# Optimization experiments

Hardware: AMD Instinct MI355X
Metric: run time of the kernel (lower is better)

## Reference

```python
import jax, jax.numpy as jnp
import numpy as np

N_NODES = 50000
N_EDGES = 300000
HEADS = 2
OUT_CH = 128
BN_EPS = 1e-5
NEG_SLOPE = 0.2


def _batchnorm(x, g, b):
    # training-mode BatchNorm1d: biased batch statistics
    mean = x.mean(axis=0)
    var = x.var(axis=0)
    return (x - mean) * jax.lax.rsqrt(var + BN_EPS) * g + b


def _gatv2(x, src, dst, edge_attr, Wl, bl, Wr, br, We, att, bias, concat):
    # PyG GATv2Conv, share_weights=False, aggr='add'
    n = x.shape[0]
    xl = (x @ Wl + bl).reshape(n, HEADS, OUT_CH)  # source messages
    xr = (x @ Wr + br).reshape(n, HEADS, OUT_CH)  # destination term
    ee = (edge_attr @ We).reshape(-1, HEADS, OUT_CH)
    s = jax.nn.leaky_relu(xl[src] + xr[dst] + ee, NEG_SLOPE)  # [E,H,C]
    alpha = jnp.einsum('ehc,hc->eh', s, att)  # [E,H]
    # segment softmax over edges grouped by destination node
    m = jax.ops.segment_max(alpha, dst, num_segments=n)
    a = jnp.exp(alpha - m[dst])
    den = jax.ops.segment_sum(a, dst, num_segments=n)
    a = a / (den[dst] + 1e-16)
    out = jax.ops.segment_sum(xl[src] * a[:, :, None], dst, num_segments=n)  # [N,H,C]
    out = out.reshape(n, HEADS * OUT_CH) if concat else out.mean(axis=1)
    return out + bias


def setup_inputs() -> dict:
    key = jax.random.key(0)
    ks = jax.random.split(key, 16)
    d = {}
    d['h'] = jax.random.normal(ks[0], (N_NODES, 5), jnp.float32)
    d['edge_index'] = jax.random.randint(ks[1], (2, N_EDGES), 0, N_NODES, jnp.int64)
    d['edge_weight'] = jax.random.uniform(ks[2], (N_EDGES, 1), jnp.float32)
    d['bn0_g'] = jnp.ones((5,), jnp.float32)
    d['bn0_b'] = jnp.zeros((5,), jnp.float32)
    d['bn1_g'] = jnp.ones((256,), jnp.float32)
    d['bn1_b'] = jnp.zeros((256,), jnp.float32)
    def lin(k, fan_in, fan_out):
        return jax.random.normal(k, (fan_in, fan_out), jnp.float32) * (1.0 / np.sqrt(fan_in))
    # conv1: in=5 -> heads*out=256, concat=True
    d['c1_Wl'] = lin(ks[3], 5, 256); d['c1_bl'] = jnp.zeros((256,), jnp.float32)
    d['c1_Wr'] = lin(ks[4], 5, 256); d['c1_br'] = jnp.zeros((256,), jnp.float32)
    d['c1_We'] = lin(ks[5], 1, 256)
    d['c1_att'] = jax.random.normal(ks[6], (HEADS, OUT_CH), jnp.float32) * 0.1
    d['c1_bias'] = jnp.zeros((256,), jnp.float32)
    # mu: in=256 -> 128, concat=False
    d['mu_Wl'] = lin(ks[7], 256, 256); d['mu_bl'] = jnp.zeros((256,), jnp.float32)
    d['mu_Wr'] = lin(ks[8], 256, 256); d['mu_br'] = jnp.zeros((256,), jnp.float32)
    d['mu_We'] = lin(ks[9], 1, 256)
    d['mu_att'] = jax.random.normal(ks[10], (HEADS, OUT_CH), jnp.float32) * 0.1
    d['mu_bias'] = jnp.zeros((128,), jnp.float32)
    # log_std: same shapes as mu
    d['ls_Wl'] = lin(ks[11], 256, 256); d['ls_bl'] = jnp.zeros((256,), jnp.float32)
    d['ls_Wr'] = lin(ks[12], 256, 256); d['ls_br'] = jnp.zeros((256,), jnp.float32)
    d['ls_We'] = lin(ks[13], 1, 256)
    d['ls_att'] = jax.random.normal(ks[14], (HEADS, OUT_CH), jnp.float32) * 0.1
    d['ls_bias'] = jnp.zeros((128,), jnp.float32)
    return d


def reference(h, edge_index, edge_weight, bn0_g, bn0_b, bn1_g, bn1_b,
              c1_Wl, c1_bl, c1_Wr, c1_br, c1_We, c1_att, c1_bias,
              mu_Wl, mu_bl, mu_Wr, mu_br, mu_We, mu_att, mu_bias,
              ls_Wl, ls_bl, ls_Wr, ls_br, ls_We, ls_att, ls_bias):
    src, dst = edge_index[0], edge_index[1]
    x = _batchnorm(h, bn0_g, bn0_b)
    x = _gatv2(x, src, dst, edge_weight, c1_Wl, c1_bl, c1_Wr, c1_br, c1_We, c1_att, c1_bias, concat=True)
    x = jax.nn.relu(_batchnorm(x, bn1_g, bn1_b))
    # dropout identity (eval / deterministic)
    mu = _gatv2(x, src, dst, edge_weight, mu_Wl, mu_bl, mu_Wr, mu_br, mu_We, mu_att, mu_bias, concat=False)
    log_std = _gatv2(x, src, dst, edge_weight, ls_Wl, ls_bl, ls_Wr, ls_br, ls_We, ls_att, ls_bias, concat=False)
    return (mu, log_std)
```

## Files before the change

### kernel.cpp

```cpp
#include <hip/hip_runtime.h>
#include <math.h>

#define N_NODES 50000
#define N_EDGES 300000
#define BN_EPS 1e-5f
#define NEG_SLOPE 0.2f

#define RB_COUNT 3128
#define SCAN_TILES 49
#define BN1_BLOCKS 523
#define K5_BLOCKS 1024

#define PREP_BN0 128
#define PREP_EC  1172
#define PREP_PW  128

typedef short bf8v __attribute__((ext_vector_type(8)));
typedef float f4v __attribute__((ext_vector_type(4)));
typedef float f2v __attribute__((ext_vector_type(2)));

__device__ inline unsigned short f2bf(float f) {
    union { float f; unsigned u; } c; c.f = f;
    unsigned r = c.u + 0x7fffu + ((c.u >> 16) & 1u);
    return (unsigned short)(r >> 16);
}

__device__ inline f2v bfpair(unsigned u) {
    union { unsigned u; float f; } lo, hi;
    lo.u = u << 16;
    hi.u = u & 0xffff0000u;
    f2v r; r.x = lo.f; r.y = hi.f;
    return r;
}

__device__ inline void async_copy16(void* lds, const void* g) {
    __builtin_amdgcn_global_load_lds(
        (const __attribute__((address_space(1))) unsigned int*)g,
        (__attribute__((address_space(3))) unsigned int*)lds, 16, 0, 0);
}

__global__ __launch_bounds__(256) void prep(
        const float* __restrict__ h, float* __restrict__ acc,
        const int* __restrict__ dst, int* __restrict__ count,
        const float* __restrict__ Wl0, const float* __restrict__ Wr0,
        const float* __restrict__ Wl1, const float* __restrict__ Wr1,
        unsigned short* __restrict__ bp) {
    int b = blockIdx.x;
    if (b < PREP_BN0) {
        __shared__ float lds[4][10];
        int tid = threadIdx.x;
        int lane = tid & 63, wave = tid >> 6;
        float ls[5] = {0,0,0,0,0}, lq[5] = {0,0,0,0,0};
        for (int r = b * 256 + tid; r < N_NODES; r += PREP_BN0 * 256) {
            #pragma unroll
            for (int k = 0; k < 5; k++) {
                float v = h[r*5 + k];
                ls[k] += v; lq[k] += v*v;
            }
        }
        #pragma unroll
        for (int k = 0; k < 5; k++) {
            #pragma unroll
            for (int m = 1; m <= 32; m <<= 1) {
                ls[k] += __shfl_xor(ls[k], m, 64);
                lq[k] += __shfl_xor(lq[k], m, 64);
            }
        }
        if (lane == 0) {
            #pragma unroll
            for (int k = 0; k < 5; k++) { lds[wave][k] = ls[k]; lds[wave][5+k] = lq[k]; }
        }
        __syncthreads();
        if (tid < 10) {
            float s = lds[0][tid] + lds[1][tid] + lds[2][tid] + lds[3][tid];
            atomicAdd(&acc[tid], s);
        }
    } else if (b < PREP_BN0 + PREP_EC) {
        int e = (b - PREP_BN0) * 256 + threadIdx.x;
        if (e < N_EDGES) atomicAdd(&count[dst[e]], 1);
    } else {
        int t = (b - PREP_BN0 - PREP_EC) * 256 + threadIdx.x;
        int lane = t & 63;
        int nt = (t >> 6) & 31;
        int kc = (t >> 11) & 7;
        int conv = t >> 14;
        int col = nt * 16 + (lane & 15);
        int k0 = kc * 32 + (lane >> 4) * 8;
        const float* W = conv ? (col < 256 ? Wl1 : Wr1) : (col < 256 ? Wl0 : Wr0);
        int c = col & 255;
        union { unsigned short h[8]; uint4 u; } tmp;
        #pragma unroll
        for (int j = 0; j < 8; j++) tmp.h[j] = f2bf(W[(size_t)(k0 + j) * 256 + c]);
        *reinterpret_cast<uint4*>(bp + (size_t)t * 8) = tmp.u;
    }
}

__global__ void local_scan(const int* __restrict__ count, int* __restrict__ offsets,
                           int* __restrict__ tileSum) {
    __shared__ int wsum[16];
    int tid = threadIdx.x;
    int lane = tid & 63, wv = tid >> 6;
    int i = blockIdx.x * 1024 + tid;
    int v = (i < N_NODES) ? count[i] : 0;
    int inc = v;
    #pragma unroll
    for (int off = 1; off < 64; off <<= 1) {
        int t = __shfl_up(inc, off, 64);
        if (lane >= off) inc += t;
    }
    if (lane == 63) wsum[wv] = inc;
    __syncthreads();
    if (wv == 0) {
        int val = (lane < 16) ? wsum[lane] : 0;
        int inc2 = val;
        #pragma unroll
        for (int off = 1; off < 16; off <<= 1) {
            int t = __shfl_up(inc2, off, 64);
            if (lane >= off) inc2 += t;
        }
        if (lane < 16) wsum[lane] = inc2 - val;
    }
    __syncthreads();
    int excl = inc - v + wsum[wv];
    if (i < N_NODES) offsets[i] = excl;
    if (tid == 1023) tileSum[blockIdx.x] = excl + v;
}

__global__ void add_prefix(int* __restrict__ offsets, const int* __restrict__ tileSum,
                           int* __restrict__ cursor) {
    __shared__ int spref;
    int tid = threadIdx.x;
    if (tid < 64) {
        int v = (tid < blockIdx.x) ? tileSum[tid] : 0;
        #pragma unroll
        for (int m = 1; m <= 32; m <<= 1) v += __shfl_xor(v, m, 64);
        if (tid == 0) spref = v;
    }
    __syncthreads();
    int i = blockIdx.x * 1024 + tid;
    if (i < N_NODES) {
        int o = offsets[i] + spref;
        offsets[i] = o;
        cursor[i] = o;
    }
    if (blockIdx.x == 0 && tid == 0) offsets[N_NODES] = N_EDGES;
}

__global__ void edge_scatter(const int* __restrict__ dst, const int* __restrict__ src,
                             const float* __restrict__ ew, int* __restrict__ cursor,
                             int2* __restrict__ sep) {
    int e = blockIdx.x * blockDim.x + threadIdx.x;
    if (e < N_EDGES) {
        int pos = atomicAdd(&cursor[dst[e]], 1);
        sep[pos] = make_int2(src[e], __float_as_int(ew[e]));
    }
}

__global__ __launch_bounds__(128) void gemm_k5(const float* __restrict__ h,
        const float* __restrict__ acc10, const float* __restrict__ g5,
        const float* __restrict__ b5,
        const float* __restrict__ Wl, const float* __restrict__ bl,
        const float* __restrict__ Wr, const float* __restrict__ br,
        unsigned short* __restrict__ xl, unsigned short* __restrict__ xr) {
    int c = threadIdx.x * 2;
    float sc[5], sh[5];
    #pragma unroll
    for (int k = 0; k < 5; k++) {
        float mean = acc10[k] * (1.f / N_NODES);
        float var  = acc10[5 + k] * (1.f / N_NODES) - mean * mean;
        float s = g5[k] * rsqrtf(var + BN_EPS);
        sc[k] = s; sh[k] = b5[k] - mean * s;
    }
    float wl0[5], wl1[5], wr0[5], wr1[5];
    #pragma unroll
    for (int k = 0; k < 5; k++) {
        wl0[k] = Wl[k*256 + c]; wl1[k] = Wl[k*256 + c + 1];
        wr0[k] = Wr[k*256 + c]; wr1[k] = Wr[k*256 + c + 1];
    }
    float bl0 = bl[c], bl1 = bl[c+1], br0 = br[c], br1 = br[c+1];
    int n = blockIdx.x;
    float hv[5];
    if (n < N_NODES) {
        #pragma unroll
        for (int k = 0; k < 5; k++) hv[k] = h[n*5 + k];
    }
    for (; n < N_NODES; n += K5_BLOCKS) {
        int n2 = n + K5_BLOCKS;
        float hn[5] = {0,0,0,0,0};
        if (n2 < N_NODES) {
            #pragma unroll
            for (int k = 0; k < 5; k++) hn[k] = h[n2*5 + k];
        }
        float l0 = bl0, l1 = bl1, r0 = br0, r1 = br1;
        #pragma unroll
        for (int k = 0; k < 5; k++) {
            float a = hv[k] * sc[k] + sh[k];
            l0 += a * wl0[k]; l1 += a * wl1[k];
            r0 += a * wr0[k]; r1 += a * wr1[k];
        }
        unsigned lp = (unsigned)f2bf(l0) | ((unsigned)f2bf(l1) << 16);
        unsigned rp = (unsigned)f2bf(r0) | ((unsigned)f2bf(r1) << 16);
        *reinterpret_cast<unsigned*>(xl + (size_t)n*256 + c) = lp;
        *reinterpret_cast<unsigned*>(xr + (size_t)n*256 + c) = rp;
        #pragma unroll
        for (int k = 0; k < 5; k++) hv[k] = hn[k];
    }
}

__global__ void pack_x_bn(const unsigned short* __restrict__ xh, const float* __restrict__ ss1,
                          unsigned short* __restrict__ ap) {
    int t = blockIdx.x * 256 + threadIdx.x;
    int lane = t & 63;
    int kc = (t >> 6) & 7;
    int rb = t >> 9;
    int row = rb * 16 + (lane & 15);
    int k0 = kc * 32 + (lane >> 4) * 8;
    union { unsigned short h[8]; uint4 u; } tmp;
    if (row < N_NODES) {
        uint4 u = *(const uint4*)(xh + (size_t)row * 256 + k0);
        float f[8];
        f2v p;
        p = bfpair(u.x); f[0] = p.x; f[1] = p.y;
        p = bfpair(u.y); f[2] = p.x; f[3] = p.y;
        p = bfpair(u.z); f[4] = p.x; f[5] = p.y;
        p = bfpair(u.w); f[6] = p.x; f[7] = p.y;
        #pragma unroll
        for (int j = 0; j < 8; j++) {
            int cc = k0 + j;
            float v = f[j] * ss1[cc] + ss1[256 + cc];
            v = v > 0.f ? v : 0.f;
            tmp.h[j] = f2bf(v);
        }
    } else {
        #pragma unroll
        for (int j = 0; j < 8; j++) tmp.h[j] = 0;
    }
    *reinterpret_cast<uint4*>(ap + (size_t)t * 8) = tmp.u;
}

__global__ __launch_bounds__(512) void gemm_mfma(const unsigned short* __restrict__ ap,
        const unsigned short* __restrict__ bp,
        const float* __restrict__ bl0, const float* __restrict__ br0,
        const float* __restrict__ bl1, const float* __restrict__ br1,
        unsigned short* __restrict__ xlA, unsigned short* __restrict__ xrA,
        unsigned short* __restrict__ xlB, unsigned short* __restrict__ xrB) {
    __shared__ unsigned short Bs[2][32][512];
    int cv = blockIdx.x >= 782;
    int bb = cv ? blockIdx.x - 782 : blockIdx.x;
    int lane = threadIdx.x & 63;
    int wave = threadIdx.x >> 6;
    int h = wave & 1;
    int rb = bb * 4 + (wave >> 1);

    const unsigned short* aptr = ap + (size_t)rb * 4096 + lane * 8;
    const unsigned short* bsrc = bp + (size_t)cv * 131072 + lane * 8;

    auto stage = [&](int buf, int kc) {
        #pragma unroll
        for (int j = 0; j < 4; j++) {
            int f = wave * 4 + j;
            async_copy16(&Bs[buf][f][lane * 8], bsrc + (size_t)kc * 16384 + f * 512);
        }
    };
    stage(0, 0);

    bf8v a[8];
    #pragma unroll
    for (int kc = 0; kc < 8; kc++) a[kc] = *reinterpret_cast<const bf8v*>(aptr + kc * 512);

    f4v acc[16];
    #pragma unroll
    for (int t = 0; t < 16; t++) acc[t] = (f4v){0.f, 0.f, 0.f, 0.f};

    for (int kc = 0; kc < 8; kc++) {
        __syncthreads();
        if (kc < 7) stage((kc + 1) & 1, kc + 1);
        const unsigned short* bb2 = &Bs[kc & 1][h * 16][lane * 8];
        #pragma unroll
        for (int t = 0; t < 16; t++) {
            bf8v b = *reinterpret_cast<const bf8v*>(bb2 + t * 512);
            acc[t] = __builtin_amdgcn_mfma_f32_16x16x32_bf16(a[kc], b, acc[t], 0, 0, 0);
        }
    }

    int c15 = lane & 15;
    int row0 = rb * 16 + (lane >> 4) * 4;
    unsigned short* outp = cv ? (h ? xrB : xlB) : (h ? xrA : xlA);
    const float* bias = cv ? (h ? br1 : bl1) : (h ? br0 : bl0);
    #pragma unroll
    for (int t = 0; t < 16; t++) {
        int col = t * 16 + c15;
        float bv = bias[col];
        #pragma unroll
        for (int r = 0; r < 4; r++) {
            int row = row0 + r;
            if (row < N_NODES) outp[(size_t)row * 256 + col] = f2bf(acc[t][r] + bv);
        }
    }
}

__global__ __launch_bounds__(256) void agg_concat(
        const unsigned short* __restrict__ xl, const unsigned short* __restrict__ xr,
        const float* __restrict__ We, const float* __restrict__ att,
        const int* __restrict__ offsets, const int2* __restrict__ sep,
        const float* __restrict__ bias,
        unsigned short* __restrict__ outh) {
    int n = blockIdx.x * 4 + (threadIdx.x >> 6);
    int lane = threadIdx.x & 63;
    int half = lane >> 5;
    int sub  = lane & 31;
    int cb   = (sub >> 4) * 128 + (sub & 15) * 8;
    f2v wv[4], av[4], rv[4];
    {
        f4v t0 = *(const f4v*)(We + cb);
        f4v t1 = *(const f4v*)(We + cb + 4);
        wv[0] = (f2v){t0.x, t0.y}; wv[1] = (f2v){t0.z, t0.w};
        wv[2] = (f2v){t1.x, t1.y}; wv[3] = (f2v){t1.z, t1.w};
        t0 = *(const f4v*)(att + cb);
        t1 = *(const f4v*)(att + cb + 4);
        av[0] = (f2v){t0.x, t0.y}; av[1] = (f2v){t0.z, t0.w};
        av[2] = (f2v){t1.x, t1.y}; av[3] = (f2v){t1.z, t1.w};
        uint4 r8 = *(const uint4*)(xr + ((size_t)n << 8) + cb);
        rv[0] = bfpair(r8.x); rv[1] = bfpair(r8.y);
        rv[2] = bfpair(r8.z); rv[3] = bfpair(r8.w);
    }
    int beg = offsets[n], end = offsets[n + 1];
    float den = 0.f;
    f2v acc[4];
    #pragma unroll
    for (int j = 0; j < 4; j++) acc[j] = (f2v){0.f, 0.f};

    int i = beg + half;
    float wN = 0.f;
    int2 seP = make_int2(0, 0);
    uint4 lN = {0u, 0u, 0u, 0u};
    if (i < end) {
        int2 se = sep[i];
        wN = __int_as_float(se.y);
        lN = *(const uint4*)(xl + ((size_t)se.x << 8) + cb);
    }
    if (i + 2 < end) seP = sep[i + 2];
    for (; i < end; i += 2) {
        uint4 l8 = lN; float w = wN;
        if (i + 2 < end) {
            lN = *(const uint4*)(xl + ((size_t)seP.x << 8) + cb);
            wN = __int_as_float(seP.y);
        }
        if (i + 4 < end) seP = sep[i + 4];
        f2v w2 = (f2v){w, w};
        f2v lv[4];
        lv[0] = bfpair(l8.x); lv[1] = bfpair(l8.y);
        lv[2] = bfpair(l8.z); lv[3] = bfpair(l8.w);
        f2v da = (f2v){0.f, 0.f};
        #pragma unroll
        for (int j = 0; j < 4; j++) {
            f2v v = lv[j] + rv[j] + w2 * wv[j];
            f2v s = v * (f2v){NEG_SLOPE, NEG_SLOPE};
            v.x = fmaxf(v.x, s.x); v.y = fmaxf(v.y, s.y);
            da += v * av[j];
        }
        float a = da.x + da.y;
        a += __shfl_xor(a, 1, 64);
        a += __shfl_xor(a, 2, 64);
        a += __shfl_xor(a, 4, 64);
        a += __shfl_xor(a, 8, 64);
        float p = __expf(a);
        den += p;
        f2v p2 = (f2v){p, p};
        #pragma unroll
        for (int j = 0; j < 4; j++) acc[j] += p2 * lv[j];
    }
    den += __shfl_xor(den, 32, 64);
    #pragma unroll
    for (int j = 0; j < 4; j++) {
        f2v ao;
        ao.x = __shfl_xor(acc[j].x, 32, 64);
        ao.y = __shfl_xor(acc[j].y, 32, 64);
        acc[j] += ao;
    }
    float inv = 1.f / (den + 1e-16f);
    if (lane < 32) {
        union { unsigned short hh[8]; uint4 u; } o;
        #pragma unroll
        for (int j = 0; j < 4; j++) {
            o.hh[2*j]   = f2bf(acc[j].x * inv + bias[cb + 2*j]);
            o.hh[2*j+1] = f2bf(acc[j].y * inv + bias[cb + 2*j + 1]);
        }
        *(uint4*)(outh + (size_t)n * 256 + cb) = o.u;
    }
}

__global__ __launch_bounds__(256) void agg_dual(
        const unsigned short* __restrict__ xlA, const unsigned short* __restrict__ xrA,
        const unsigned short* __restrict__ xlB, const unsigned short* __restrict__ xrB,
        const float* __restrict__ WeA, const float* __restrict__ attA,
        const float* __restrict__ WeB, const float* __restrict__ attB,
        const int* __restrict__ offsets, const int2* __restrict__ sep,
        const float* __restrict__ biasA, const float* __restrict__ biasB,
        float* __restrict__ outA, float* __restrict__ outB) {
    int n = blockIdx.x * 4 + (threadIdx.x >> 6);
    int lane = threadIdx.x & 63;
    int half = lane >> 5;
    int sub  = lane & 31;
    int cb   = (sub >> 4) * 128 + (sub & 15) * 8;
    f2v wvA[4], avA[4], rvA[4], wvB[4], avB[4], rvB[4];
    {
        f4v t0 = *(const f4v*)(WeA + cb);
        f4v t1 = *(const f4v*)(WeA + cb + 4);
        wvA[0] = (f2v){t0.x, t0.y}; wvA[1] = (f2v){t0.z, t0.w};
        wvA[2] = (f2v){t1.x, t1.y}; wvA[3] = (f2v){t1.z, t1.w};
        t0 = *(const f4v*)(attA + cb);
        t1 = *(const f4v*)(attA + cb + 4);
        avA[0] = (f2v){t0.x, t0.y}; avA[1] = (f2v){t0.z, t0.w};
        avA[2] = (f2v){t1.x, t1.y}; avA[3] = (f2v){t1.z, t1.w};
        t0 = *(const f4v*)(WeB + cb);
        t1 = *(const f4v*)(WeB + cb + 4);
        wvB[0] = (f2v){t0.x, t0.y}; wvB[1] = (f2v){t0.z, t0.w};
        wvB[2] = (f2v){t1.x, t1.y}; wvB[3] = (f2v){t1.z, t1.w};
        t0 = *(const f4v*)(attB + cb);
        t1 = *(const f4v*)(attB + cb + 4);
        avB[0] = (f2v){t0.x, t0.y}; avB[1] = (f2v){t0.z, t0.w};
        avB[2] = (f2v){t1.x, t1.y}; avB[3] = (f2v){t1.z, t1.w};
        uint4 r8 = *(const uint4*)(xrA + ((size_t)n << 8) + cb);
        rvA[0] = bfpair(r8.x); rvA[1] = bfpair(r8.y);
        rvA[2] = bfpair(r8.z); rvA[3] = bfpair(r8.w);
        r8 = *(const uint4*)(xrB + ((size_t)n << 8) + cb);
        rvB[0] = bfpair(r8.x); rvB[1] = bfpair(r8.y);
        rvB[2] = bfpair(r8.z); rvB[3] = bfpair(r8.w);
    }
    int beg = offsets[n], end = offsets[n + 1];
    float dA = 0.f, dB = 0.f;
    f2v accA[4], accB[4];
    #pragma unroll
    for (int j = 0; j < 4; j++) { accA[j] = (f2v){0.f, 0.f}; accB[j] = (f2v){0.f, 0.f}; }

    int i = beg + half;
    float wN = 0.f;
    int2 seP = make_int2(0, 0);
    uint4 lNA = {0u, 0u, 0u, 0u}, lNB = {0u, 0u, 0u, 0u};
    if (i < end) {
        int2 se = sep[i];
        wN = __int_as_float(se.y);
        size_t o = ((size_t)se.x << 8) + cb;
        lNA = *(const uint4*)(xlA + o);
        lNB = *(const uint4*)(xlB + o);
    }
    if (i + 2 < end) seP = sep[i + 2];
    for (; i < end; i += 2) {
        uint4 lA = lNA, lB = lNB; float w = wN;
        if (i + 2 < end) {
            size_t o = ((size_t)seP.x << 8) + cb;
            lNA = *(const uint4*)(xlA + o);
            lNB = *(const uint4*)(xlB + o);
            wN = __int_as_float(seP.y);
        }
        if (i + 4 < end) seP = sep[i + 4];
        f2v w2 = (f2v){w, w};
        f2v lvA[4], lvB[4];
        lvA[0] = bfpair(lA.x); lvA[1] = bfpair(lA.y);
        lvA[2] = bfpair(lA.z); lvA[3] = bfpair(lA.w);
        lvB[0] = bfpair(lB.x); lvB[1] = bfpair(lB.y);
        lvB[2] = bfpair(lB.z); lvB[3] = bfpair(lB.w);
        f2v daA = (f2v){0.f, 0.f}, daB = (f2v){0.f, 0.f};
        #pragma unroll
        for (int j = 0; j < 4; j++) {
            f2v vA = lvA[j] + rvA[j] + w2 * wvA[j];
            f2v sA = vA * (f2v){NEG_SLOPE, NEG_SLOPE};
            vA.x = fmaxf(vA.x, sA.x); vA.y = fmaxf(vA.y, sA.y);
            daA += vA * avA[j];
            f2v vB = lvB[j] + rvB[j] + w2 * wvB[j];
            f2v sB = vB * (f2v){NEG_SLOPE, NEG_SLOPE};
            vB.x = fmaxf(vB.x, sB.x); vB.y = fmaxf(vB.y, sB.y);
            daB += vB * avB[j];
        }
        float aA = daA.x + daA.y, aB = daB.x + daB.y;
        float tA, tB;
        tA = __shfl_xor(aA, 1, 64); tB = __shfl_xor(aB, 1, 64); aA += tA; aB += tB;
        tA = __shfl_xor(aA, 2, 64); tB = __shfl_xor(aB, 2, 64); aA += tA; aB += tB;
        tA = __shfl_xor(aA, 4, 64); tB = __shfl_xor(aB, 4, 64); aA += tA; aB += tB;
        tA = __shfl_xor(aA, 8, 64); tB = __shfl_xor(aB, 8, 64); aA += tA; aB += tB;
        float pA = __expf(aA), pB = __expf(aB);
        dA += pA; dB += pB;
        f2v pA2 = (f2v){pA, pA}, pB2 = (f2v){pB, pB};
        #pragma unroll
        for (int j = 0; j < 4; j++) {
            accA[j] += pA2 * lvA[j];
            accB[j] += pB2 * lvB[j];
        }
    }
    dA += __shfl_xor(dA, 32, 64);
    dB += __shfl_xor(dB, 32, 64);
    #pragma unroll
    for (int j = 0; j < 4; j++) {
        f2v ao;
        ao.x = __shfl_xor(accA[j].x, 32, 64);
        ao.y = __shfl_xor(accA[j].y, 32, 64);
        accA[j] += ao;
        ao.x = __shfl_xor(accB[j].x, 32, 64);
        ao.y = __shfl_xor(accB[j].y, 32, 64);
        accB[j] += ao;
    }
    float invA = 1.f / (dA + 1e-16f);
    float invB = 1.f / (dB + 1e-16f);
    float oA[8], oB[8], poA[8], poB[8];
    #pragma unroll
    for (int j = 0; j < 4; j++) {
        oA[2*j]   = accA[j].x * invA;
        oA[2*j+1] = accA[j].y * invA;
        oB[2*j]   = accB[j].x * invB;
        oB[2*j+1] = accB[j].y * invB;
    }
    #pragma unroll
    for (int j = 0; j < 8; j++) {
        poA[j] = __shfl_xor(oA[j], 16, 64);
        poB[j] = __shfl_xor(oB[j], 16, 64);
    }
    int q = lane >> 4;
    int c0 = (lane & 15) * 8;
    if (q == 0) {
        float r[8];
        #pragma unroll
        for (int j = 0; j < 8; j++) r[j] = (oA[j] + poA[j]) * 0.5f + biasA[c0 + j];
        *(float4*)(outA + (size_t)n * 128 + c0)     = *(float4*)&r[0];
        *(float4*)(outA + (size_t)n * 128 + c0 + 4) = *(float4*)&r[4];
    } else if (q == 2) {
        float r[8];
        #pragma unroll
        for (int j = 0; j < 8; j++) r[j] = (oB[j] + poB[j]) * 0.5f + biasB[c0 + j];
        *(float4*)(outB + (size_t)n * 128 + c0)     = *(float4*)&r[0];
        *(float4*)(outB + (size_t)n * 128 + c0 + 4) = *(float4*)&r[4];
    }
}

__global__ void bn1_reduce(const unsigned short* __restrict__ xh, float* __restrict__ part) {
    __shared__ float lds[256][9];
    int tid = threadIdx.x;
    int cg = tid & 63;
    int ph = tid >> 6;
    int r0 = blockIdx.x * 96;
    float s[4] = {0,0,0,0}, q[4] = {0,0,0,0};
    #pragma unroll
    for (int it = 0; it < 24; it++) {
        int row = r0 + it * 4 + ph;
        if (row < N_NODES) {
            uint2 v = *(const uint2*)(xh + (size_t)row * 256 + cg * 4);
            f2v p0 = bfpair(v.x), p1 = bfpair(v.y);
            s[0] += p0.x; s[1] += p0.y; s[2] += p1.x; s[3] += p1.y;
            q[0] += p0.x*p0.x; q[1] += p0.y*p0.y; q[2] += p1.x*p1.x; q[3] += p1.y*p1.y;
        }
    }
    #pragma unroll
    for (int j = 0; j < 4; j++) { lds[tid][j] = s[j]; lds[tid][4+j] = q[j]; }
    __syncthreads();
    if (tid < 64) {
        float4 sv, qv;
        float* svp = (float*)&sv; float* qvp = (float*)&qv;
        #pragma unroll
        for (int j = 0; j < 4; j++) {
            svp[j] = lds[tid][j] + lds[tid+64][j] + lds[tid+128][j] + lds[tid+192][j];
            qvp[j] = lds[tid][4+j] + lds[tid+64][4+j] + lds[tid+128][4+j] + lds[tid+192][4+j];
        }
        *(float4*)(part + (size_t)blockIdx.x * 512 + cg * 4) = sv;
        *(float4*)(part + (size_t)blockIdx.x * 512 + 256 + cg * 4) = qv;
    }
}

__global__ void bn1_finalize(const float* __restrict__ part, const float* __restrict__ g,
                             const float* __restrict__ b, float* __restrict__ ss1) {
    __shared__ float lds[8][64];
    int t = threadIdx.x;
    int c = blockIdx.x * 32 + (t & 31);
    int ph = t >> 5;
    float s = 0.f, q = 0.f;
    for (int bi = ph; bi < BN1_BLOCKS; bi += 8) {
        s += part[(size_t)bi * 512 + c];
        q += part[(size_t)bi * 512 + 256 + c];
    }
    lds[ph][t & 31] = s;
    lds[ph][32 + (t & 31)] = q;
    __syncthreads();
    if (t < 32) {
        float ss = 0.f, qq = 0.f;
        #pragma unroll
        for (int p = 0; p < 8; p++) { ss += lds[p][t]; qq += lds[p][32 + t]; }
        float mean = ss * (1.f / N_NODES);
        float var  = qq * (1.f / N_NODES) - mean * mean;
        float sc = g[c] * rsqrtf(var + BN_EPS);
        ss1[c] = sc;
        ss1[256 + c] = b[c] - mean * sc;
    }
}

extern "C" void kernel_launch(void* const* d_in, const int* in_sizes, int n_in,
                              void* d_out, int out_size, void* d_ws, size_t ws_size,
                              hipStream_t stream) {
    const float* h          = (const float*)d_in[0];
    const int*   edge_index = (const int*)d_in[1];
    const int*   src = edge_index;
    const int*   dst = edge_index + N_EDGES;
    const float* ew   = (const float*)d_in[2];
    const float* bn0g = (const float*)d_in[3];
    const float* bn0b = (const float*)d_in[4];
    const float* bn1g = (const float*)d_in[5];
    const float* bn1b = (const float*)d_in[6];
    const float* c1_Wl = (const float*)d_in[7];
    const float* c1_bl = (const float*)d_in[8];
    const float* c1_Wr = (const float*)d_in[9];
    const float* c1_br = (const float*)d_in[10];
    const float* c1_We = (const float*)d_in[11];
    const float* c1_att = (const float*)d_in[12];
    const float* c1_bias = (const float*)d_in[13];
    const float* mu_Wl = (const float*)d_in[14];
    const float* mu_bl = (const float*)d_in[15];
    const float* mu_Wr = (const float*)d_in[16];
    const float* mu_br = (const float*)d_in[17];
    const float* mu_We = (const float*)d_in[18];
    const float* mu_att = (const float*)d_in[19];
    const float* mu_bias = (const float*)d_in[20];
    const float* ls_Wl = (const float*)d_in[21];
    const float* ls_bl = (const float*)d_in[22];
    const float* ls_Wr = (const float*)d_in[23];
    const float* ls_br = (const float*)d_in[24];
    const float* ls_We = (const float*)d_in[25];
    const float* ls_att = (const float*)d_in[26];
    const float* ls_bias = (const float*)d_in[27];

    float* out_mu = (float*)d_out;
    float* out_ls = (float*)d_out + (size_t)N_NODES * 128;

    char* ws = (char*)d_ws;
    size_t off = 0;
    auto alloc = [&](size_t bytes) -> void* {
        void* p = ws + off;
        off += (bytes + 255) / 256 * 256;
        return p;
    };
    unsigned short* xl = (unsigned short*)alloc((size_t)N_NODES * 256 * 2);
    unsigned short* xr = (unsigned short*)alloc((size_t)N_NODES * 256 * 2);
    unsigned short* xBh = (unsigned short*)alloc((size_t)N_NODES * 256 * 2);
    unsigned short* xr2 = (unsigned short*)alloc((size_t)N_NODES * 256 * 2);
    float* bn0acc  = (float*)alloc(10 * 4);
    float* bn1part = (float*)alloc((size_t)BN1_BLOCKS * 512 * 4);
    float* bn1ss   = (float*)alloc(512 * 4);
    int*   count   = (int*)alloc((size_t)N_NODES * 4);
    int*   offsets = (int*)alloc((size_t)(N_NODES + 1) * 4);
    int*   cursor  = (int*)alloc((size_t)N_NODES * 4);
    int2*  sep     = (int2*)alloc((size_t)N_EDGES * 8);
    int*   tileSum = (int*)alloc((size_t)SCAN_TILES * 4);
    unsigned short* Apack = (unsigned short*)alloc((size_t)RB_COUNT * 4096 * 2);
    unsigned short* Bpack = (unsigned short*)alloc((size_t)2 * 131072 * 2);

    unsigned short* xl2 = xBh;

    hipMemsetAsync(count, 0, (size_t)N_NODES * 4, stream);
    hipMemsetAsync(bn0acc, 0, 10 * 4, stream);

    prep<<<PREP_BN0 + PREP_EC + PREP_PW, 256, 0, stream>>>(
        h, bn0acc, dst, count, mu_Wl, mu_Wr, ls_Wl, ls_Wr, Bpack);

    local_scan<<<SCAN_TILES, 1024, 0, stream>>>(count, offsets, tileSum);
    add_prefix<<<SCAN_TILES, 1024, 0, stream>>>(offsets, tileSum, cursor);
    edge_scatter<<<(N_EDGES + 255) / 256, 256, 0, stream>>>(dst, src, ew, cursor, sep);

    gemm_k5<<<K5_BLOCKS, 128, 0, stream>>>(h, bn0acc, bn0g, bn0b,
                                           c1_Wl, c1_bl, c1_Wr, c1_br, xl, xr);
    agg_concat<<<N_NODES / 4, 256, 0, stream>>>(xl, xr, c1_We, c1_att, offsets,
                                                sep, c1_bias, xBh);

    bn1_reduce<<<BN1_BLOCKS, 256, 0, stream>>>(xBh, bn1part);
    bn1_finalize<<<8, 256, 0, stream>>>(bn1part, bn1g, bn1b, bn1ss);
    pack_x_bn<<<6256, 256, 0, stream>>>(xBh, bn1ss, Apack);

    gemm_mfma<<<1564, 512, 0, stream>>>(Apack, Bpack,
                                        mu_bl, mu_br, ls_bl, ls_br,
                                        xl, xr, xl2, xr2);

    agg_dual<<<N_NODES / 4, 256, 0, stream>>>(xl, xr, xl2, xr2,
                                              mu_We, mu_att, ls_We, ls_att,
                                              offsets, sep,
                                              mu_bias, ls_bias, out_mu, out_ls);
}
```

Measured before the change: 418.1 us.

## Fuse BN1+ReLU packing into MFMA GEMM and make aggregation kernels persistent

Removes the pack_x_bn kernel and its Apack buffer. The GEMM now reads the bf16 hidden activations directly, applies the BN1 scale/shift and ReLU in registers to build the A fragments, and computes both the mu and log_std projections in a single block so each A tile is loaded once. The aggregation kernels switch to a grid-stride persistent form with 2048 blocks, hoisting the bias loads and prefetching the next node's offsets. Because xl2 no longer aliases xBh it gets its own allocation, which uses more workspace. Halving the GEMM grid also lowers parallelism.

```diff
diff --git a/kernel.cpp b/kernel.cpp
--- a/kernel.cpp
+++ b/kernel.cpp
@@ -10,6 +10,9 @@
 #define SCAN_TILES 49
 #define BN1_BLOCKS 523
 #define K5_BLOCKS 1024
+
+#define AGG_BLOCKS 2048
+#define AGG_STRIDE (AGG_BLOCKS * 4)
 
 #define PREP_BN0 128
 #define PREP_EC  1172
@@ -207,94 +210,94 @@
     }
 }
 
-__global__ void pack_x_bn(const unsigned short* __restrict__ xh, const float* __restrict__ ss1,
-                          unsigned short* __restrict__ ap) {
-    int t = blockIdx.x * 256 + threadIdx.x;
-    int lane = t & 63;
-    int kc = (t >> 6) & 7;
-    int rb = t >> 9;
-    int row = rb * 16 + (lane & 15);
-    int k0 = kc * 32 + (lane >> 4) * 8;
-    union { unsigned short h[8]; uint4 u; } tmp;
-    if (row < N_NODES) {
-        uint4 u = *(const uint4*)(xh + (size_t)row * 256 + k0);
-        float f[8];
-        f2v p;
-        p = bfpair(u.x); f[0] = p.x; f[1] = p.y;
-        p = bfpair(u.y); f[2] = p.x; f[3] = p.y;
-        p = bfpair(u.z); f[4] = p.x; f[5] = p.y;
-        p = bfpair(u.w); f[6] = p.x; f[7] = p.y;
-        #pragma unroll
-        for (int j = 0; j < 8; j++) {
-            int cc = k0 + j;
-            float v = f[j] * ss1[cc] + ss1[256 + cc];
-            v = v > 0.f ? v : 0.f;
-            tmp.h[j] = f2bf(v);
-        }
-    } else {
-        #pragma unroll
-        for (int j = 0; j < 8; j++) tmp.h[j] = 0;
-    }
-    *reinterpret_cast<uint4*>(ap + (size_t)t * 8) = tmp.u;
-}
-
-__global__ __launch_bounds__(512) void gemm_mfma(const unsigned short* __restrict__ ap,
+__global__ __launch_bounds__(512) void gemm_mfma(const unsigned short* __restrict__ xh,
+        const float* __restrict__ ss1,
         const unsigned short* __restrict__ bp,
         const float* __restrict__ bl0, const float* __restrict__ br0,
         const float* __restrict__ bl1, const float* __restrict__ br1,
         unsigned short* __restrict__ xlA, unsigned short* __restrict__ xrA,
         unsigned short* __restrict__ xlB, unsigned short* __restrict__ xrB) {
     __shared__ unsigned short Bs[2][32][512];
-    int cv = blockIdx.x >= 782;
-    int bb = cv ? blockIdx.x - 782 : blockIdx.x;
     int lane = threadIdx.x & 63;
     int wave = threadIdx.x >> 6;
     int h = wave & 1;
-    int rb = bb * 4 + (wave >> 1);
-
-    const unsigned short* aptr = ap + (size_t)rb * 4096 + lane * 8;
-    const unsigned short* bsrc = bp + (size_t)cv * 131072 + lane * 8;
-
-    auto stage = [&](int buf, int kc) {
-        #pragma unroll
-        for (int j = 0; j < 4; j++) {
-            int f = wave * 4 + j;
-            async_copy16(&Bs[buf][f][lane * 8], bsrc + (size_t)kc * 16384 + f * 512);
-        }
-    };
-    stage(0, 0);
-
+    int rb = blockIdx.x * 4 + (wave >> 1);
+
+    int row = rb * 16 + (lane & 15);
+    int k0b = (lane >> 4) * 8;
+    bool rok = row < N_NODES;
     bf8v a[8];
     #pragma unroll
-    for (int kc = 0; kc < 8; kc++) a[kc] = *reinterpret_cast<const bf8v*>(aptr + kc * 512);
-
-    f4v acc[16];
-    #pragma unroll
-    for (int t = 0; t < 16; t++) acc[t] = (f4v){0.f, 0.f, 0.f, 0.f};
-
     for (int kc = 0; kc < 8; kc++) {
-        __syncthreads();
-        if (kc < 7) stage((kc + 1) & 1, kc + 1);
-        const unsigned short* bb2 = &Bs[kc & 1][h * 16][lane * 8];
-        #pragma unroll
-        for (int t = 0; t < 16; t++) {
-            bf8v b = *reinterpret_cast<const bf8v*>(bb2 + t * 512);
-            acc[t] = __builtin_amdgcn_mfma_f32_16x16x32_bf16(a[kc], b, acc[t], 0, 0, 0);
-        }
+        int k0 = kc * 32 + k0b;
+        union { unsigned short hh[8]; uint4 u; bf8v v; } tmp;
+        if (rok) {
+            uint4 u = *(const uint4*)(xh + (size_t)row * 256 + k0);
+            f4v s0 = *(const f4v*)(ss1 + k0);
+            f4v s1 = *(const f4v*)(ss1 + k0 + 4);
+            f4v h0 = *(const f4v*)(ss1 + 256 + k0);
+            f4v h1 = *(const f4v*)(ss1 + 256 + k0 + 4);
+            float f[8];
+            f2v p;
+            p = bfpair(u.x); f[0] = p.x; f[1] = p.y;
+            p = bfpair(u.y); f[2] = p.x; f[3] = p.y;
+            p = bfpair(u.z); f[4] = p.x; f[5] = p.y;
+            p = bfpair(u.w); f[6] = p.x; f[7] = p.y;
+            float scv[8] = {s0.x, s0.y, s0.z, s0.w, s1.x, s1.y, s1.z, s1.w};
+            float shv[8] = {h0.x, h0.y, h0.z, h0.w, h1.x, h1.y, h1.z, h1.w};
+            #pragma unroll
+            for (int j = 0; j < 8; j++) {
+                float v = f[j] * scv[j] + shv[j];
+                v = v > 0.f ? v : 0.f;
+                tmp.hh[j] = f2bf(v);
+            }
+        } else {
+            tmp.u = (uint4){0u, 0u, 0u, 0u};
+        }
+        a[kc] = tmp.v;
     }
 
     int c15 = lane & 15;
     int row0 = rb * 16 + (lane >> 4) * 4;
-    unsigned short* outp = cv ? (h ? xrB : xlB) : (h ? xrA : xlA);
-    const float* bias = cv ? (h ? br1 : bl1) : (h ? br0 : bl0);
+
     #pragma unroll
-    for (int t = 0; t < 16; t++) {
-        int col = t * 16 + c15;
-        float bv = bias[col];
-        #pragma unroll
-        for (int r = 0; r < 4; r++) {
-            int row = row0 + r;
-            if (row < N_NODES) outp[(size_t)row * 256 + col] = f2bf(acc[t][r] + bv);
+    for (int cv = 0; cv < 2; cv++) {
+        const unsigned short* bsrc = bp + (size_t)cv * 131072 + lane * 8;
+        auto stage = [&](int buf, int kc) {
+            #pragma unroll
+            for (int j = 0; j < 4; j++) {
+                int f = wave * 4 + j;
+                async_copy16(&Bs[buf][f][lane * 8], bsrc + (size_t)kc * 16384 + f * 512);
+            }
+        };
+        stage(0, 0);
+
+        f4v acc[16];
+        #pragma unroll
+        for (int t = 0; t < 16; t++) acc[t] = (f4v){0.f, 0.f, 0.f, 0.f};
+
+        for (int kc = 0; kc < 8; kc++) {
+            __syncthreads();
+            if (kc < 7) stage((kc + 1) & 1, kc + 1);
+            const unsigned short* bb2 = &Bs[kc & 1][h * 16][lane * 8];
+            #pragma unroll
+            for (int t = 0; t < 16; t++) {
+                bf8v b = *reinterpret_cast<const bf8v*>(bb2 + t * 512);
+                acc[t] = __builtin_amdgcn_mfma_f32_16x16x32_bf16(a[kc], b, acc[t], 0, 0, 0);
+            }
+        }
+
+        unsigned short* outp = cv ? (h ? xrB : xlB) : (h ? xrA : xlA);
+        const float* bias = cv ? (h ? br1 : bl1) : (h ? br0 : bl0);
+        #pragma unroll
+        for (int t = 0; t < 16; t++) {
+            int col = t * 16 + c15;
+            float bv = bias[col];
+            #pragma unroll
+            for (int r = 0; r < 4; r++) {
+                int rr = row0 + r;
+                if (rr < N_NODES) outp[(size_t)rr * 256 + col] = f2bf(acc[t][r] + bv);
+            }
         }
     }
 }
@@ -305,12 +308,13 @@
         const int* __restrict__ offsets, const int2* __restrict__ sep,
         const float* __restrict__ bias,
         unsigned short* __restrict__ outh) {
-    int n = blockIdx.x * 4 + (threadIdx.x >> 6);
+    int gw = blockIdx.x * 4 + (threadIdx.x >> 6);
     int lane = threadIdx.x & 63;
     int half = lane >> 5;
     int sub  = lane & 31;
     int cb   = (sub >> 4) * 128 + (sub & 15) * 8;
-    f2v wv[4], av[4], rv[4];
+    f2v wv[4], av[4];
+    float bs[8];
     {
         f4v t0 = *(const f4v*)(We + cb);
         f4v t1 = *(const f4v*)(We + cb + 4);
@@ -320,73 +324,87 @@
         t1 = *(const f4v*)(att + cb + 4);
         av[0] = (f2v){t0.x, t0.y}; av[1] = (f2v){t0.z, t0.w};
         av[2] = (f2v){t1.x, t1.y}; av[3] = (f2v){t1.z, t1.w};
+        t0 = *(const f4v*)(bias + cb);
+        t1 = *(const f4v*)(bias + cb + 4);
+        bs[0]=t0.x; bs[1]=t0.y; bs[2]=t0.z; bs[3]=t0.w;
+        bs[4]=t1.x; bs[5]=t1.y; bs[6]=t1.z; bs[7]=t1.w;
+    }
+    int n = gw;
+    int beg = 0, end = 0;
+    if (n < N_NODES) { beg = offsets[n]; end = offsets[n + 1]; }
+    while (n < N_NODES) {
+        int nn = n + AGG_STRIDE;
+        int nbeg = 0, nend = 0;
+        if (nn < N_NODES) { nbeg = offsets[nn]; nend = offsets[nn + 1]; }
         uint4 r8 = *(const uint4*)(xr + ((size_t)n << 8) + cb);
+        f2v rv[4];
         rv[0] = bfpair(r8.x); rv[1] = bfpair(r8.y);
         rv[2] = bfpair(r8.z); rv[3] = bfpair(r8.w);
-    }
-    int beg = offsets[n], end = offsets[n + 1];
-    float den = 0.f;
-    f2v acc[4];
-    #pragma unroll
-    for (int j = 0; j < 4; j++) acc[j] = (f2v){0.f, 0.f};
-
-    int i = beg + half;
-    float wN = 0.f;
-    int2 seP = make_int2(0, 0);
-    uint4 lN = {0u, 0u, 0u, 0u};
-    if (i < end) {
-        int2 se = sep[i];
-        wN = __int_as_float(se.y);
-        lN = *(const uint4*)(xl + ((size_t)se.x << 8) + cb);
-    }
-    if (i + 2 < end) seP = sep[i + 2];
-    for (; i < end; i += 2) {
-        uint4 l8 = lN; float w = wN;
-        if (i + 2 < end) {
-            lN = *(const uint4*)(xl + ((size_t)seP.x << 8) + cb);
-            wN = __int_as_float(seP.y);
-        }
-        if (i + 4 < end) seP = sep[i + 4];
-        f2v w2 = (f2v){w, w};
-        f2v lv[4];
-        lv[0] = bfpair(l8.x); lv[1] = bfpair(l8.y);
-        lv[2] = bfpair(l8.z); lv[3] = bfpair(l8.w);
-        f2v da = (f2v){0.f, 0.f};
+
+        float den = 0.f;
+        f2v acc[4];
+        #pragma unroll
+        for (int j = 0; j < 4; j++) acc[j] = (f2v){0.f, 0.f};
+
+        int i = beg + half;
+        float wN = 0.f;
+        int2 seP = make_int2(0, 0);
+        uint4 lN = {0u, 0u, 0u, 0u};
+        if (i < end) {
+            int2 se = sep[i];
+            wN = __int_as_float(se.y);
+            lN = *(const uint4*)(xl + ((size_t)se.x << 8) + cb);
+        }
+        if (i + 2 < end) seP = sep[i + 2];
+        for (; i < end; i += 2) {
+            uint4 l8 = lN; float w = wN;
+            if (i + 2 < end) {
+                lN = *(const uint4*)(xl + ((size_t)seP.x << 8) + cb);
+                wN = __int_as_float(seP.y);
+            }
+            if (i + 4 < end) seP = sep[i + 4];
+            f2v w2 = (f2v){w, w};
+            f2v lv[4];
+            lv[0] = bfpair(l8.x); lv[1] = bfpair(l8.y);
+            lv[2] = bfpair(l8.z); lv[3] = bfpair(l8.w);
+            f2v da = (f2v){0.f, 0.f};
+            #pragma unroll
+            for (int j = 0; j < 4; j++) {
+                f2v v = lv[j] + rv[j] + w2 * wv[j];
+                f2v s = v * (f2v){NEG_SLOPE, NEG_SLOPE};
+                v.x = fmaxf(v.x, s.x); v.y = fmaxf(v.y, s.y);
+                da += v * av[j];
+            }
+            float a = da.x + da.y;
+            a += __shfl_xor(a, 1, 64);
+            a += __shfl_xor(a, 2, 64);
+            a += __shfl_xor(a, 4, 64);
+            a += __shfl_xor(a, 8, 64);
+            float p = __expf(a);
+            den += p;
+            f2v p2 = (f2v){p, p};
+            #pragma unroll
+            for (int j = 0; j < 4; j++) acc[j] += p2 * lv[j];
+        }
+        den += __shfl_xor(den, 32, 64);
         #pragma unroll
         for (int j = 0; j < 4; j++) {
-            f2v v = lv[j] + rv[j] + w2 * wv[j];
-            f2v s = v * (f2v){NEG_SLOPE, NEG_SLOPE};
-            v.x = fmaxf(v.x, s.x); v.y = fmaxf(v.y, s.y);
-            da += v * av[j];
-        }
-        float a = da.x + da.y;
-        a += __shfl_xor(a, 1, 64);
-        a += __shfl_xor(a, 2, 64);
-        a += __shfl_xor(a, 4, 64);
-        a += __shfl_xor(a, 8, 64);
-        float p = __expf(a);
-        den += p;
-        f2v p2 = (f2v){p, p};
-        #pragma unroll
-        for (int j = 0; j < 4; j++) acc[j] += p2 * lv[j];
-    }
-    den += __shfl_xor(den, 32, 64);
-    #pragma unroll
-    for (int j = 0; j < 4; j++) {
-        f2v ao;
-        ao.x = __shfl_xor(acc[j].x, 32, 64);
-        ao.y = __shfl_xor(acc[j].y, 32, 64);
-        acc[j] += ao;
-    }
-    float inv = 1.f / (den + 1e-16f);
-    if (lane < 32) {
-        union { unsigned short hh[8]; uint4 u; } o;
-        #pragma unroll
-        for (int j = 0; j < 4; j++) {
-            o.hh[2*j]   = f2bf(acc[j].x * inv + bias[cb + 2*j]);
-            o.hh[2*j+1] = f2bf(acc[j].y * inv + bias[cb + 2*j + 1]);
-        }
-        *(uint4*)(outh + (size_t)n * 256 + cb) = o.u;
+            f2v ao;
+            ao.x = __shfl_xor(acc[j].x, 32, 64);
+            ao.y = __shfl_xor(acc[j].y, 32, 64);
+            acc[j] += ao;
+        }
+        float inv = 1.f / (den + 1e-16f);
+        if (lane < 32) {
+            union { unsigned short hh[8]; uint4 u; } o;
+            #pragma unroll
+            for (int j = 0; j < 4; j++) {
+                o.hh[2*j]   = f2bf(acc[j].x * inv + bs[2*j]);
+                o.hh[2*j+1] = f2bf(acc[j].y * inv + bs[2*j + 1]);
+            }
+            *(uint4*)(outh + (size_t)n * 256 + cb) = o.u;
+        }
+        n = nn; beg = nbeg; end = nend;
     }
 }
 
@@ -398,12 +416,14 @@
         const int* __restrict__ offsets, const int2* __restrict__ sep,
         const float* __restrict__ biasA, const float* __restrict__ biasB,
         float* __restrict__ outA, float* __restrict__ outB) {
-    int n = blockIdx.x * 4 + (threadIdx.x >> 6);
+    int gw = blockIdx.x * 4 + (threadIdx.x >> 6);
     int lane = threadIdx.x & 63;
     int half = lane >> 5;
     int sub  = lane & 31;
     int cb   = (sub >> 4) * 128 + (sub & 15) * 8;
-    f2v wvA[4], avA[4], rvA[4], wvB[4], avB[4], rvB[4];
+    int c0 = (lane & 15) * 8;
+    f2v wvA[4], avA[4], wvB[4], avB[4];
+    float bsv[8];
     {
         f4v t0 = *(const f4v*)(WeA + cb);
         f4v t1 = *(const f4v*)(WeA + cb + 4);
@@ -421,114 +441,128 @@
         t1 = *(const f4v*)(attB + cb + 4);
         avB[0] = (f2v){t0.x, t0.y}; avB[1] = (f2v){t0.z, t0.w};
         avB[2] = (f2v){t1.x, t1.y}; avB[3] = (f2v){t1.z, t1.w};
-        uint4 r8 = *(const uint4*)(xrA + ((size_t)n << 8) + cb);
-        rvA[0] = bfpair(r8.x); rvA[1] = bfpair(r8.y);
-        rvA[2] = bfpair(r8.z); rvA[3] = bfpair(r8.w);
-        r8 = *(const uint4*)(xrB + ((size_t)n << 8) + cb);
-        rvB[0] = bfpair(r8.x); rvB[1] = bfpair(r8.y);
-        rvB[2] = bfpair(r8.z); rvB[3] = bfpair(r8.w);
-    }
-    int beg = offsets[n], end = offsets[n + 1];
-    float dA = 0.f, dB = 0.f;
-    f2v accA[4], accB[4];
-    #pragma unroll
-    for (int j = 0; j < 4; j++) { accA[j] = (f2v){0.f, 0.f}; accB[j] = (f2v){0.f, 0.f}; }
-
-    int i = beg + half;
-    float wN = 0.f;
-    int2 seP = make_int2(0, 0);
-    uint4 lNA = {0u, 0u, 0u, 0u}, lNB = {0u, 0u, 0u, 0u};
-    if (i < end) {
-        int2 se = sep[i];
-        wN = __int_as_float(se.y);
-        size_t o = ((size_t)se.x << 8) + cb;
-        lNA = *(const uint4*)(xlA + o);
-        lNB = *(const uint4*)(xlB + o);
-    }
-    if (i + 2 < end) seP = sep[i + 2];
-    for (; i < end; i += 2) {
-        uint4 lA = lNA, lB = lNB; float w = wN;
-        if (i + 2 < end) {
-            size_t o = ((size_t)seP.x << 8) + cb;
+        const float* bp = (lane < 32) ? biasA : biasB;
+        f4v b0 = *(const f4v*)(bp + c0);
+        f4v b1 = *(const f4v*)(bp + c0 + 4);
+        bsv[0]=b0.x; bsv[1]=b0.y; bsv[2]=b0.z; bsv[3]=b0.w;
+        bsv[4]=b1.x; bsv[5]=b1.y; bsv[6]=b1.z; bsv[7]=b1.w;
+    }
+    int n = gw;
+    int beg = 0, end = 0;
+    if (n < N_NODES) { beg = offsets[n]; end = offsets[n + 1]; }
+    while (n < N_NODES) {
+        int nn = n + AGG_STRIDE;
+        int nbeg = 0, nend = 0;
+        if (nn < N_NODES) { nbeg = offsets[nn]; nend = offsets[nn + 1]; }
+        uint4 r8A = *(const uint4*)(xrA + ((size_t)n << 8) + cb);
+        uint4 r8B = *(const uint4*)(xrB + ((size_t)n << 8) + cb);
+        f2v rvA[4], rvB[4];
+        rvA[0] = bfpair(r8A.x); rvA[1] = bfpair(r8A.y);
+        rvA[2] = bfpair(r8A.z); rvA[3] = bfpair(r8A.w);
+        rvB[0] = bfpair(r8B.x); rvB[1] = bfpair(r8B.y);
+        rvB[2] = bfpair(r8B.z); rvB[3] = bfpair(r8B.w);
+
+        float dA = 0.f, dB = 0.f;
+        f2v accA[4], accB[4];
+        #pragma unroll
+        for (int j = 0; j < 4; j++) { accA[j] = (f2v){0.f, 0.f}; accB[j] = (f2v){0.f, 0.f}; }
+
+        int i = beg + half;
+        float wN = 0.f;
+        int2 seP = make_int2(0, 0);
+        uint4 lNA = {0u, 0u, 0u, 0u}, lNB = {0u, 0u, 0u, 0u};
+        if (i < end) {
+            int2 se = sep[i];
+            wN = __int_as_float(se.y);
+            size_t o = ((size_t)se.x << 8) + cb;
             lNA = *(const uint4*)(xlA + o);
             lNB = *(const uint4*)(xlB + o);
-            wN = __int_as_float(seP.y);
-        }
-        if (i + 4 < end) seP = sep[i + 4];
-        f2v w2 = (f2v){w, w};
-        f2v lvA[4], lvB[4];
-        lvA[0] = bfpair(lA.x); lvA[1] = bfpair(lA.y);
-        lvA[2] = bfpair(lA.z); lvA[3] = bfpair(lA.w);
-        lvB[0] = bfpair(lB.x); lvB[1] = bfpair(lB.y);
-        lvB[2] = bfpair(lB.z); lvB[3] = bfpair(lB.w);
-        f2v daA = (f2v){0.f, 0.f}, daB = (f2v){0.f, 0.f};
+        }
+        if (i + 2 < end) seP = sep[i + 2];
+        for (; i < end; i += 2) {
+            uint4 lA = lNA, lB = lNB; float w = wN;
+            if (i + 2 < end) {
+                size_t o = ((size_t)seP.x << 8) + cb;
+                lNA = *(const uint4*)(xlA + o);
+                lNB = *(const uint4*)(xlB + o);
+                wN = __int_as_float(seP.y);
+            }
+            if (i + 4 < end) seP = sep[i + 4];
+            f2v w2 = (f2v){w, w};
+            f2v lvA[4], lvB[4];
+            lvA[0] = bfpair(lA.x); lvA[1] = bfpair(lA.y);
+            lvA[2] = bfpair(lA.z); lvA[3] = bfpair(lA.w);
+            lvB[0] = bfpair(lB.x); lvB[1] = bfpair(lB.y);
+            lvB[2] = bfpair(lB.z); lvB[3] = bfpair(lB.w);
+            f2v daA = (f2v){0.f, 0.f}, daB = (f2v){0.f, 0.f};
+            #pragma unroll
+            for (int j = 0; j < 4; j++) {
+                f2v vA = lvA[j] + rvA[j] + w2 * wvA[j];
+                f2v sA = vA * (f2v){NEG_SLOPE, NEG_SLOPE};
+                vA.x = fmaxf(vA.x, sA.x); vA.y = fmaxf(vA.y, sA.y);
+                daA += vA * avA[j];
+                f2v vB = lvB[j] + rvB[j] + w2 * wvB[j];
+                f2v sB = vB * (f2v){NEG_SLOPE, NEG_SLOPE};
+                vB.x = fmaxf(vB.x, sB.x); vB.y = fmaxf(vB.y, sB.y);
+                daB += vB * avB[j];
+            }
+            float aA = daA.x + daA.y, aB = daB.x + daB.y;
+            float tA, tB;
+            tA = __shfl_xor(aA, 1, 64); tB = __shfl_xor(aB, 1, 64); aA += tA; aB += tB;
+            tA = __shfl_xor(aA, 2, 64); tB = __shfl_xor(aB, 2, 64); aA += tA; aB += tB;
+            tA = __shfl_xor(aA, 4, 64); tB = __shfl_xor(aB, 4, 64); aA += tA; aB += tB;
+            tA = __shfl_xor(aA, 8, 64); tB = __shfl_xor(aB, 8, 64); aA += tA; aB += tB;
+            float pA = __expf(aA), pB = __expf(aB);
+            dA += pA; dB += pB;
+            f2v pA2 = (f2v){pA, pA}, pB2 = (f2v){pB, pB};
+            #pragma unroll
+            for (int j = 0; j < 4; j++) {
+                accA[j] += pA2 * lvA[j];
+                accB[j] += pB2 * lvB[j];
+            }
+        }
+        dA += __shfl_xor(dA, 32, 64);
+        dB += __shfl_xor(dB, 32, 64);
         #pragma unroll
         for (int j = 0; j < 4; j++) {
-            f2v vA = lvA[j] + rvA[j] + w2 * wvA[j];
-            f2v sA = vA * (f2v){NEG_SLOPE, NEG_SLOPE};
-            vA.x = fmaxf(vA.x, sA.x); vA.y = fmaxf(vA.y, sA.y);
-            daA += vA * avA[j];
-            f2v vB = lvB[j] + rvB[j] + w2 * wvB[j];
-            f2v sB = vB * (f2v){NEG_SLOPE, NEG_SLOPE};
-            vB.x = fmaxf(vB.x, sB.x); vB.y = fmaxf(vB.y, sB.y);
-            daB += vB * avB[j];
-        }
-        float aA = daA.x + daA.y, aB = daB.x + daB.y;
-        float tA, tB;
-        tA = __shfl_xor(aA, 1, 64); tB = __shfl_xor(aB, 1, 64); aA += tA; aB += tB;
-        tA = __shfl_xor(aA, 2, 64); tB = __shfl_xor(aB, 2, 64); aA += tA; aB += tB;
-        tA = __shfl_xor(aA, 4, 64); tB = __shfl_xor(aB, 4, 64); aA += tA; aB += tB;
-        tA = __shfl_xor(aA, 8, 64); tB = __shfl_xor(aB, 8, 64); aA += tA; aB += tB;
-        float pA = __expf(aA), pB = __expf(aB);
-        dA += pA; dB += pB;
-        f2v pA2 = (f2v){pA, pA}, pB2 = (f2v){pB, pB};
+            f2v ao;
+            ao.x = __shfl_xor(accA[j].x, 32, 64);
+            ao.y = __shfl_xor(accA[j].y, 32, 64);
+            accA[j] += ao;
+            ao.x = __shfl_xor(accB[j].x, 32, 64);
+            ao.y = __shfl_xor(accB[j].y, 32, 64);
+            accB[j] += ao;
+        }
+        float invA = 1.f / (dA + 1e-16f);
+        float invB = 1.f / (dB + 1e-16f);
+        float oA[8], oB[8], poA[8], poB[8];
         #pragma unroll
         for (int j = 0; j < 4; j++) {
-            accA[j] += pA2 * lvA[j];
-            accB[j] += pB2 * lvB[j];
-        }
-    }
-    dA += __shfl_xor(dA, 32, 64);
-    dB += __shfl_xor(dB, 32, 64);
-    #pragma unroll
-    for (int j = 0; j < 4; j++) {
-        f2v ao;
-        ao.x = __shfl_xor(accA[j].x, 32, 64);
-        ao.y = __shfl_xor(accA[j].y, 32, 64);
-        accA[j] += ao;
-        ao.x = __shfl_xor(accB[j].x, 32, 64);
-        ao.y = __shfl_xor(accB[j].y, 32, 64);
-        accB[j] += ao;
-    }
-    float invA = 1.f / (dA + 1e-16f);
-    float invB = 1.f / (dB + 1e-16f);
-    float oA[8], oB[8], poA[8], poB[8];
-    #pragma unroll
-    for (int j = 0; j < 4; j++) {
-        oA[2*j]   = accA[j].x * invA;
-        oA[2*j+1] = accA[j].y * invA;
-        oB[2*j]   = accB[j].x * invB;
-        oB[2*j+1] = accB[j].y * invB;
-    }
-    #pragma unroll
-    for (int j = 0; j < 8; j++) {
-        poA[j] = __shfl_xor(oA[j], 16, 64);
-        poB[j] = __shfl_xor(oB[j], 16, 64);
-    }
-    int q = lane >> 4;
-    int c0 = (lane & 15) * 8;
-    if (q == 0) {
-        float r[8];
-        #pragma unroll
-        for (int j = 0; j < 8; j++) r[j] = (oA[j] + poA[j]) * 0.5f + biasA[c0 + j];
-        *(float4*)(outA + (size_t)n * 128 + c0)     = *(float4*)&r[0];
-        *(float4*)(outA + (size_t)n * 128 + c0 + 4) = *(float4*)&r[4];
-    } else if (q == 2) {
-        float r[8];
-        #pragma unroll
-        for (int j = 0; j < 8; j++) r[j] = (oB[j] + poB[j]) * 0.5f + biasB[c0 + j];
-        *(float4*)(outB + (size_t)n * 128 + c0)     = *(float4*)&r[0];
-        *(float4*)(outB + (size_t)n * 128 + c0 + 4) = *(float4*)&r[4];
+            oA[2*j]   = accA[j].x * invA;
+            oA[2*j+1] = accA[j].y * invA;
+            oB[2*j]   = accB[j].x * invB;
+            oB[2*j+1] = accB[j].y * invB;
+        }
+        #pragma unroll
+        for (int j = 0; j < 8; j++) {
+            poA[j] = __shfl_xor(oA[j], 16, 64);
+            poB[j] = __shfl_xor(oB[j], 16, 64);
+        }
+        int q = lane >> 4;
+        if (q == 0) {
+            float r[8];
+            #pragma unroll
+            for (int j = 0; j < 8; j++) r[j] = (oA[j] + poA[j]) * 0.5f + bsv[j];
+            *(float4*)(outA + (size_t)n * 128 + c0)     = *(float4*)&r[0];
+            *(float4*)(outA + (size_t)n * 128 + c0 + 4) = *(float4*)&r[4];
+        } else if (q == 2) {
+            float r[8];
+            #pragma unroll
+            for (int j = 0; j < 8; j++) r[j] = (oB[j] + poB[j]) * 0.5f + bsv[j];
+            *(float4*)(outB + (size_t)n * 128 + c0)     = *(float4*)&r[0];
+            *(float4*)(outB + (size_t)n * 128 + c0 + 4) = *(float4*)&r[4];
+        }
+        n = nn; beg = nbeg; end = nend;
     }
 }
 
@@ -635,9 +669,10 @@
         off += (bytes + 255) / 256 * 256;
         return p;
     };
-    unsigned short* xl = (unsigned short*)alloc((size_t)N_NODES * 256 * 2);
-    unsigned short* xr = (unsigned short*)alloc((size_t)N_NODES * 256 * 2);
+    unsigned short* xl  = (unsigned short*)alloc((size_t)N_NODES * 256 * 2);
+    unsigned short* xr  = (unsigned short*)alloc((size_t)N_NODES * 256 * 2);
     unsigned short* xBh = (unsigned short*)alloc((size_t)N_NODES * 256 * 2);
+    unsigned short* xl2 = (unsigned short*)alloc((size_t)N_NODES * 256 * 2);
     unsigned short* xr2 = (unsigned short*)alloc((size_t)N_NODES * 256 * 2);
     float* bn0acc  = (float*)alloc(10 * 4);
     float* bn1part = (float*)alloc((size_t)BN1_BLOCKS * 512 * 4);
@@ -647,10 +682,7 @@
     int*   cursor  = (int*)alloc((size_t)N_NODES * 4);
     int2*  sep     = (int2*)alloc((size_t)N_EDGES * 8);
     int*   tileSum = (int*)alloc((size_t)SCAN_TILES * 4);
-    unsigned short* Apack = (unsigned short*)alloc((size_t)RB_COUNT * 4096 * 2);
     unsigned short* Bpack = (unsigned short*)alloc((size_t)2 * 131072 * 2);
-
-    unsigned short* xl2 = xBh;
 
     hipMemsetAsync(count, 0, (size_t)N_NODES * 4, stream);
     hipMemsetAsync(bn0acc, 0, 10 * 4, stream);
@@ -664,19 +696,18 @@
 
     gemm_k5<<<K5_BLOCKS, 128, 0, stream>>>(h, bn0acc, bn0g, bn0b,
                                            c1_Wl, c1_bl, c1_Wr, c1_br, xl, xr);
-    agg_concat<<<N_NODES / 4, 256, 0, stream>>>(xl, xr, c1_We, c1_att, offsets,
-                                                sep, c1_bias, xBh);
+    agg_concat<<<AGG_BLOCKS, 256, 0, stream>>>(xl, xr, c1_We, c1_att, offsets,
+                                               sep, c1_bias, xBh);
 
     bn1_reduce<<<BN1_BLOCKS, 256, 0, stream>>>(xBh, bn1part);
     bn1_finalize<<<8, 256, 0, stream>>>(bn1part, bn1g, bn1b, bn1ss);
-    pack_x_bn<<<6256, 256, 0, stream>>>(xBh, bn1ss, Apack);
-
-    gemm_mfma<<<1564, 512, 0, stream>>>(Apack, Bpack,
-                                        mu_bl, mu_br, ls_bl, ls_br,
-                                        xl, xr, xl2, xr2);
-
-    agg_dual<<<N_NODES / 4, 256, 0, stream>>>(xl, xr, xl2, xr2,
-                                              mu_We, mu_att, ls_We, ls_att,
-                                              offsets, sep,
-                                              mu_bias, ls_bias, out_mu, out_ls);
-}
+
+    gemm_mfma<<<782, 512, 0, stream>>>(xBh, bn1ss, Bpack,
+                                       mu_bl, mu_br, ls_bl, ls_br,
+                                       xl, xr, xl2, xr2);
+
+    agg_dual<<<AGG_BLOCKS, 256, 0, stream>>>(xl, xr, xl2, xr2,
+                                             mu_We, mu_att, ls_We, ls_att,
+                                             offsets, sep,
+                                             mu_bias, ls_bias, out_mu, out_ls);
+}
```

Measured after the change: 467.0 us. 1.12x slower.
